# Performance work log

Measured on AMD Instinct MI355X. Metric: run time of the kernel, lower is better.

The kernel has to match this reference:

```python
import jax, jax.numpy as jnp
import numpy as np

B, N, T, D, M, HOPS = 32, 300, 12, 64, 16, 2

def setup_inputs() -> dict:
    key = jax.random.key(0)
    ks = jax.random.split(key, 12)
    inp = {
        "X": jax.random.normal(ks[0], (B, D, N, T), dtype=jnp.float32),
        "timeEmbedding": jax.random.normal(ks[1], (B, N, T, D), dtype=jnp.float32),
        "adjW": jax.random.normal(ks[2], (N, D), dtype=jnp.float32) * (1.0 / np.sqrt(D)),
        "adjB": jnp.zeros((N,), dtype=jnp.float32),
        "trainW1": jax.random.normal(ks[3], (N, M), dtype=jnp.float32) * 0.1,
        "trainW2": jax.random.normal(ks[4], (M, D * D), dtype=jnp.float32) * 0.1,
        "alpha1": jax.random.normal(ks[5], (N, M), dtype=jnp.float32) * 0.1,
        "alpha2": jax.random.normal(ks[6], (M, N), dtype=jnp.float32) * 0.1,
        "beta1": jax.random.normal(ks[7], (N, M), dtype=jnp.float32) * 0.1,
        "beta2": jax.random.normal(ks[8], (M, N), dtype=jnp.float32) * 0.1,
        "gcnW": jax.random.normal(ks[9], (D, D * (HOPS + 1)), dtype=jnp.float32) * (1.0 / np.sqrt(D * (HOPS + 1))),
        "gcnB": jnp.zeros((D,), dtype=jnp.float32),
    }
    return inp

def reference(X, timeEmbedding, adjW, adjB, trainW1, trainW2, alpha1, alpha2, beta1, beta2, gcnW, gcnB):
    # timeEmbedding: [B,N,T,D] -> [B,T,N,D]
    te = jnp.transpose(timeEmbedding, (0, 2, 1, 3))
    # learned adjacency: A[b,t,n,k]
    A = jnp.sin(jnp.einsum('btnd,kd->btnk', te, adjW) + adjB)  # Linear(dmodel->N)
    A = (alpha1 @ alpha2) * A            # elementwise scale by [N,N], broadcast over b,t
    A = jax.nn.relu(A + beta1 @ beta2)
    # X: [B,D,N,T] -> [B,T,N,D]
    Xp = jnp.transpose(X, (0, 3, 2, 1))
    # per-node weight matrices [N,D,D]
    W = (trainW1 @ trainW2).reshape(N, D, D)
    Hs = [Xp]
    Hb = Xp
    for _ in range(HOPS):
        Hnow = jnp.einsum('btnk,btkd->btnd', A, Hb)      # adjacency aggregation
        Hnow = jnp.einsum('btnk,nkd->btnd', Hnow, W)     # per-node distinct matmul
        pre = Xp + Hnow
        Hnow = jax.nn.sigmoid(pre) * jnp.tanh(pre)        # gated residual
        Hs.append(Hnow)
        Hb = Hnow
    H = jnp.concatenate(Hs, axis=3)                       # [B,T,N,D*(hops+1)]
    Hout = jnp.einsum('btnf,df->btnd', H, gcnW) + gcnB    # gcnLinear (dropout = identity in eval)
    return jnp.transpose(Hout, (0, 3, 2, 1))              # [B,D,N,T]
```

## Files before the change

kernel.cpp:

```cpp
#include <hip/hip_runtime.h>

#define Nq 300
#define Tq 12
#define Dq 64
#define Mq 16
#define BTq 384
#define DDq (Dq*Dq)
#define Fq (Dq*3)
#define NP 320

typedef short bf8_t __attribute__((ext_vector_type(8)));
typedef float f4_t  __attribute__((ext_vector_type(4)));

__device__ __forceinline__ unsigned short f2bf(float f) {
    unsigned u = __float_as_uint(f);
    u = (u + 0x7FFFu + ((u >> 16) & 1u)) >> 16;
    return (unsigned short)u;
}
__device__ __forceinline__ float bf2f(unsigned short u) {
    return __uint_as_float((unsigned)u << 16);
}
__device__ __forceinline__ float4 ld4(const float* p) { return *(const float4*)p; }

__device__ __forceinline__ bf8_t pack8(float4 a, float4 b) {
    bf8_t r;
    r[0] = (short)f2bf(a.x); r[1] = (short)f2bf(a.y);
    r[2] = (short)f2bf(a.z); r[3] = (short)f2bf(a.w);
    r[4] = (short)f2bf(b.x); r[5] = (short)f2bf(b.y);
    r[6] = (short)f2bf(b.z); r[7] = (short)f2bf(b.w);
    return r;
}

__device__ __forceinline__ float gatef(float p) {
    float pc = fminf(fmaxf(p, -30.f), 30.f);
    float sig = 1.f / (1.f + __expf(-pc));
    float e2  = __expf(2.f * pc);
    float th  = (e2 - 1.f) / (e2 + 1.f);
    return sig * th;
}

__global__ void __launch_bounds__(256) kprep_all(
    const float* __restrict__ a1, const float* __restrict__ a2,
    const float* __restrict__ b1, const float* __restrict__ b2,
    const float* __restrict__ w1, const float* __restrict__ w2,
    const float* __restrict__ adjW, const float* __restrict__ adjB,
    const float* __restrict__ X,
    unsigned* __restrict__ ABt, unsigned short* __restrict__ Wt,
    unsigned short* __restrict__ adjWb, float* __restrict__ adjBp,
    unsigned short* __restrict__ Xp_t, unsigned short* __restrict__ Xp_nb)
{
    __shared__ char smem[64 * 308 * 2];
    const int vb = blockIdx.x;
    const int tid = threadIdx.x;

    if (vb < 400) {
        const int tile = vb;
        const int reg = tid & 3, lane = tid >> 2;
        const int nt = tile % 5;  int r1 = tile / 5;
        const int w  = r1 % 4;    int r2 = r1 / 4;
        const int c  = r2 % 5;    const int qi = r2 / 5;
        const int n = qi*80 + nt*16 + (lane & 15);
        const int k = c*64 + w*16 + (lane >> 4)*4 + reg;
        unsigned outv = 0u;
        if (n < Nq && k < Nq) {
            float sa = 0.f, sb = 0.f;
            #pragma unroll
            for (int m = 0; m < Mq; ++m) {
                sa = fmaf(a1[n*Mq+m], a2[m*Nq+k], sa);
                sb = fmaf(b1[n*Mq+m], b2[m*Nq+k], sb);
            }
            outv = ((unsigned)f2bf(sb) << 16) | (unsigned)f2bf(sa);
        }
        ABt[tile*256 + tid] = outv;
    } else if (vb < 700) {
        float* sT = (float*)smem;
        __shared__ float sw1[Mq];
        const int n = vb - 400;
        if (tid < Mq) sw1[tid] = w1[n*Mq + tid];
        __syncthreads();
        for (int i = tid; i < DDq; i += 256) {
            int k = i >> 6, d = i & 63;
            float s = 0.f;
            #pragma unroll
            for (int m = 0; m < Mq; ++m) s = fmaf(sw1[m], w2[m*DDq + i], s);
            sT[d*65 + k] = s;
        }
        __syncthreads();
        for (int i = tid; i < DDq; i += 256) {
            int d = i >> 6, k = i & 63;
            Wt[(size_t)n*DDq + i] = f2bf(sT[d*65 + k]);
        }
    } else if (vb < 780) {
        int e = (vb - 700) * 256 + tid;
        if (e < NP * 64) {
            int k = e >> 6, d = e & 63;
            adjWb[e] = (k < Nq) ? f2bf(adjW[k*Dq + d]) : (unsigned short)0;
        }
        if (e < NP) adjBp[e] = (e < Nq) ? adjB[e] : 0.f;
    } else {
        unsigned short* sT = (unsigned short*)smem;
        const int bx = vb - 780;
        const int b = bx / 24, sub = bx % 24;
        const int tile = sub >> 1, half = sub & 1;
        const int n0 = tile * 25, d0 = half * 32;
        for (int i = tid; i < 32 * 75; i += 256) {
            int dl = i / 75, jq = i - dl*75, j = jq*4;
            float4 v = ld4(&X[(size_t)(b*64 + d0 + dl)*3600 + n0*12 + j]);
            ushort4 o;
            o.x = f2bf(v.x); o.y = f2bf(v.y); o.z = f2bf(v.z); o.w = f2bf(v.w);
            *(ushort4*)&sT[dl*308 + j] = o;
        }
        __syncthreads();
        for (int wi = tid; wi < 12 * 32 * 25; wi += 256) {
            int nl = wi % 25, rem = wi / 25;
            int dl = rem & 31, t = rem >> 5;
            Xp_t[((size_t)(b*Tq + t)*64 + d0 + dl)*NP + n0 + nl] = sT[dl*308 + nl*12 + t];
        }
        if (tile == 11) {
            for (int wi = tid; wi < 12 * 32 * 20; wi += 256) {
                int e = wi % 20, rem = wi / 20;
                int dl = rem & 31, t = rem >> 5;
                Xp_t[((size_t)(b*Tq + t)*64 + d0 + dl)*NP + 300 + e] = 0;
            }
        }
        for (int wi = tid; wi < 25 * 12 * 8; wi += 256) {
            int dg = wi & 7, rem = wi >> 3;
            int t = rem % 12, nl = rem / 12;
            ushort4 o;
            o.x = sT[(dg*4+0)*308 + nl*12 + t];
            o.y = sT[(dg*4+1)*308 + nl*12 + t];
            o.z = sT[(dg*4+2)*308 + nl*12 + t];
            o.w = sT[(dg*4+3)*308 + nl*12 + t];
            *(ushort4*)&Xp_nb[((size_t)(n0+nl)*BTq + b*Tq + t)*64 + d0 + dg*4] = o;
        }
    }
}

__global__ void __launch_bounds__(256) ktr2(const unsigned short* __restrict__ Hnb,
                                            unsigned short* __restrict__ Ht) {
    __shared__ unsigned short sT[64 * 308];
    const int bt = blockIdx.x;
    const int tid = threadIdx.x;
    for (int i = tid; i < 300 * 16; i += 256) {
        int nl = i >> 4, dg = i & 15;
        ushort4 v = *(const ushort4*)&Hnb[((size_t)nl*BTq + bt)*64 + dg*4];
        sT[(dg*4+0)*308 + nl] = v.x;
        sT[(dg*4+1)*308 + nl] = v.y;
        sT[(dg*4+2)*308 + nl] = v.z;
        sT[(dg*4+3)*308 + nl] = v.w;
    }
    __syncthreads();
    for (int wi = tid; wi < 64 * 80; wi += 256) {
        int kq = wi % 80, d = wi / 80;
        ushort4 o;
        int k = kq * 4;
        o.x = (k+0 < Nq) ? sT[d*308 + k+0] : (unsigned short)0;
        o.y = (k+1 < Nq) ? sT[d*308 + k+1] : (unsigned short)0;
        o.z = (k+2 < Nq) ? sT[d*308 + k+2] : (unsigned short)0;
        o.w = (k+3 < Nq) ? sT[d*308 + k+3] : (unsigned short)0;
        *(ushort4*)&Ht[((size_t)bt*64 + d)*NP + k] = o;
    }
}

template<int HOP>
__global__ void __launch_bounds__(256) kfuse_t(
    const float* __restrict__ te,
    unsigned short* __restrict__ teP,
    const unsigned short* __restrict__ adjWb,
    const float* __restrict__ adjBp,
    const unsigned* __restrict__ ABt,
    const unsigned short* __restrict__ Hb_t,
    unsigned short* __restrict__ Hout_nb)
{
    __shared__ unsigned short sPl[2][80 * 72];
    const int bt = blockIdx.x >> 2, qi = blockIdx.x & 3;
    const int b = bt / Tq, t = bt - b * Tq;
    const int nbase = qi * 80;
    const int tid = threadIdx.x;
    const int w = tid >> 6, lane = tid & 63, quad = lane >> 4, l16 = lane & 15;
    const int dcol = w*16 + l16;

    bf8_t tb0[5], tb1[5];
    #pragma unroll
    for (int nt = 0; nt < 5; ++nt) {
        int n = nbase + nt*16 + l16; if (n > Nq-1) n = Nq-1;
        if (HOP == 1) {
            const float* ter = te + (((size_t)b*Nq + n)*Tq + t)*Dq;
            tb0[nt] = pack8(ld4(ter + quad*8),      ld4(ter + quad*8 + 4));
            tb1[nt] = pack8(ld4(ter + 32 + quad*8), ld4(ter + 36 + quad*8));
            if (w == 0) {
                *(bf8_t*)&teP[((size_t)bt*Nq + n)*64 + quad*8] = tb0[nt];
                *(bf8_t*)&teP[((size_t)bt*Nq + n)*64 + 32 + quad*8] = tb1[nt];
            }
        } else {
            const unsigned short* tr = teP + ((size_t)bt*Nq + n)*64;
            tb0[nt] = *(const bf8_t*)(tr + quad*8);
            tb1[nt] = *(const bf8_t*)(tr + 32 + quad*8);
        }
    }
    f4_t accO[5];
    #pragma unroll
    for (int rt = 0; rt < 5; ++rt) accO[rt] = (f4_t){0.f, 0.f, 0.f, 0.f};

    const unsigned short* hr = Hb_t + ((size_t)bt*64 + dcol)*NP;
    bf8_t hv0 = *(const bf8_t*)(hr + quad*8);
    bf8_t hv1 = *(const bf8_t*)(hr + 32 + quad*8);

    for (int c = 0; c < 5; ++c) {
        const int cbase = c * 64;
        bf8_t nhv0, nhv1;
        if (c < 4) {
            nhv0 = *(const bf8_t*)(hr + cbase + 64 + quad*8);
            nhv1 = *(const bf8_t*)(hr + cbase + 96 + quad*8);
        }
        const unsigned* abbase = ABt + ((((size_t)qi*5 + c)*4 + w)*5)*256 + lane*4;
        uint4 abv[5];
        #pragma unroll
        for (int nt = 0; nt < 5; ++nt) abv[nt] = *(const uint4*)(abbase + nt*256);
        const unsigned short* ar = adjWb + (cbase + w*16 + l16)*64;
        bf8_t ka0 = *(const bf8_t*)(ar + quad*8);
        bf8_t ka1 = *(const bf8_t*)(ar + 32 + quad*8);
        float4 bias4 = ld4(adjBp + cbase + w*16 + quad*4);
        unsigned short* sp = sPl[c & 1];
        #pragma unroll
        for (int nt = 0; nt < 5; ++nt) {
            f4_t p = {0.f, 0.f, 0.f, 0.f};
            p = __builtin_amdgcn_mfma_f32_16x16x32_bf16(ka0, tb0[nt], p, 0, 0, 0);
            p = __builtin_amdgcn_mfma_f32_16x16x32_bf16(ka1, tb1[nt], p, 0, 0, 0);
            uint4 ab = abv[nt];
            ushort4 o4;
            {
                float sv = __sinf(p[0] + bias4.x);
                o4.x = f2bf(fmaxf(fmaf(__uint_as_float(ab.x << 16), sv,
                                       __uint_as_float(ab.x & 0xFFFF0000u)), 0.f));
            }
            {
                float sv = __sinf(p[1] + bias4.y);
                o4.y = f2bf(fmaxf(fmaf(__uint_as_float(ab.y << 16), sv,
                                       __uint_as_float(ab.y & 0xFFFF0000u)), 0.f));
            }
            {
                float sv = __sinf(p[2] + bias4.z);
                o4.z = f2bf(fmaxf(fmaf(__uint_as_float(ab.z << 16), sv,
                                       __uint_as_float(ab.z & 0xFFFF0000u)), 0.f));
            }
            {
                float sv = __sinf(p[3] + bias4.w);
                o4.w = f2bf(fmaxf(fmaf(__uint_as_float(ab.w << 16), sv,
                                       __uint_as_float(ab.w & 0xFFFF0000u)), 0.f));
            }
            *(ushort4*)&sp[(nt*16 + l16)*72 + w*16 + quad*4] = o4;
        }
        __syncthreads();
        #pragma unroll
        for (int rt = 0; rt < 5; ++rt) {
            bf8_t p0 = *(const bf8_t*)&sp[(rt*16 + l16)*72 + quad*8];
            bf8_t p1 = *(const bf8_t*)&sp[(rt*16 + l16)*72 + 32 + quad*8];
            accO[rt] = __builtin_amdgcn_mfma_f32_16x16x32_bf16(hv0, p0, accO[rt], 0, 0, 0);
            accO[rt] = __builtin_amdgcn_mfma_f32_16x16x32_bf16(hv1, p1, accO[rt], 0, 0, 0);
        }
        if (c < 4) { hv0 = nhv0; hv1 = nhv1; }
    }
    #pragma unroll
    for (int rt = 0; rt < 5; ++rt) {
        int n = nbase + rt*16 + l16;
        if (n < Nq) {
            ushort4 o;
            o.x = f2bf(accO[rt][0]); o.y = f2bf(accO[rt][1]);
            o.z = f2bf(accO[rt][2]); o.w = f2bf(accO[rt][3]);
            *(ushort4*)&Hout_nb[((size_t)n*BTq + bt)*64 + w*16 + quad*4] = o;
        }
    }
}

__global__ void __launch_bounds__(256) kmm(
    const unsigned short* __restrict__ Hagg_nb,
    const unsigned short* __restrict__ Xp_nb,
    const unsigned short* __restrict__ Wt,
    unsigned short* __restrict__ Hout_nb)
{
    const int n = blockIdx.x >> 2, qi = blockIdx.x & 3;
    const int bt0 = qi * 96;
    const int tid = threadIdx.x;
    const int w = tid >> 6, lane = tid & 63, quad = lane >> 4, l16 = lane & 15;
    const int dcol = w*16 + l16;
    const unsigned short* wn = Wt + (size_t)n * DDq + dcol*64;
    bf8_t v0 = *(const bf8_t*)(wn + quad*8);
    bf8_t v1 = *(const bf8_t*)(wn + 32 + quad*8);
    bf8_t a0[6], a1[6];
    #pragma unroll
    for (int rt = 0; rt < 6; ++rt) {
        int r = bt0 + rt*16 + l16;
        const unsigned short* row = Hagg_nb + ((size_t)n*BTq + r)*64;
        a0[rt] = *(const bf8_t*)(row + quad*8);
        a1[rt] = *(const bf8_t*)(row + 32 + quad*8);
    }
    f4_t acc[6];
    #pragma unroll
    for (int rt = 0; rt < 6; ++rt) acc[rt] = (f4_t){0.f, 0.f, 0.f, 0.f};
    #pragma unroll
    for (int rt = 0; rt < 6; ++rt) {
        acc[rt] = __builtin_amdgcn_mfma_f32_16x16x32_bf16(v0, a0[rt], acc[rt], 0, 0, 0);
        acc[rt] = __builtin_amdgcn_mfma_f32_16x16x32_bf16(v1, a1[rt], acc[rt], 0, 0, 0);
    }
    __syncthreads();
    ushort4 xp4[6];
    #pragma unroll
    for (int rt = 0; rt < 6; ++rt) {
        int r = bt0 + rt*16 + l16;
        xp4[rt] = *(const ushort4*)&Xp_nb[((size_t)n*BTq + r)*64 + w*16 + quad*4];
    }
    #pragma unroll
    for (int rt = 0; rt < 6; ++rt) {
        int r = bt0 + rt*16 + l16;
        ushort4 o;
        o.x = f2bf(gatef(bf2f(xp4[rt].x) + acc[rt][0]));
        o.y = f2bf(gatef(bf2f(xp4[rt].y) + acc[rt][1]));
        o.z = f2bf(gatef(bf2f(xp4[rt].z) + acc[rt][2]));
        o.w = f2bf(gatef(bf2f(xp4[rt].w) + acc[rt][3]));
        *(ushort4*)&Hout_nb[((size_t)n*BTq + r)*64 + w*16 + quad*4] = o;
    }
}

__global__ void __launch_bounds__(256) kgcn(
    const unsigned short* __restrict__ Xp_nb, const unsigned short* __restrict__ H1_nb,
    const unsigned short* __restrict__ H2_nb, const float* __restrict__ gcnW,
    const float* __restrict__ gcnB, float* __restrict__ out)
{
    const int bid = blockIdx.x;
    const int b = bid / 57, rem = bid % 57;
    const int tile = rem / 3, rg = rem % 3;
    const int n0 = tile * 16;
    const int rows = (tile == 18) ? 144 : 192;
    const int r0base = rg * 64;
    const int tid = threadIdx.x;
    const int w = tid >> 6, lane = tid & 63, quad = lane >> 4, l16 = lane & 15;
    const int dcol = w*16 + l16;
    const float bias = gcnB[dcol];
    f4_t acc[4];
    #pragma unroll
    for (int rt = 0; rt < 4; ++rt) acc[rt] = (f4_t){0.f, 0.f, 0.f, 0.f};
    const unsigned short* bufs[3] = {Xp_nb, H1_nb, H2_nb};
    #pragma unroll
    for (int c = 0; c < 3; ++c) {
        const unsigned short* buf = bufs[c];
        const float* gwr = gcnW + (size_t)dcol*Fq + c*Dq;
        bf8_t v0 = pack8(ld4(gwr + quad*8),      ld4(gwr + quad*8 + 4));
        bf8_t v1 = pack8(ld4(gwr + 32 + quad*8), ld4(gwr + 36 + quad*8));
        #pragma unroll
        for (int rt = 0; rt < 4; ++rt) {
            int rr = r0base + rt*16;
            if (rr < rows) {
                int r = rr + l16;
                int nl = r / 12, t = r - nl*12;
                int n = n0 + nl; if (n > Nq-1) n = Nq-1;
                const unsigned short* row = buf + ((size_t)n*BTq + b*Tq + t)*64;
                bf8_t a0 = *(const bf8_t*)(row + quad*8);
                bf8_t a1 = *(const bf8_t*)(row + 32 + quad*8);
                acc[rt] = __builtin_amdgcn_mfma_f32_16x16x32_bf16(a0, v0, acc[rt], 0, 0, 0);
                acc[rt] = __builtin_amdgcn_mfma_f32_16x16x32_bf16(a1, v1, acc[rt], 0, 0, 0);
            }
        }
    }
    float* outd = out + (size_t)(b*Dq + dcol)*3600 + n0*12;
    #pragma unroll
    for (int rt = 0; rt < 4; ++rt) {
        int rr = r0base + rt*16;
        if (rr < rows) {
            int r0 = rr + quad*4;
            float4 o = make_float4(acc[rt][0] + bias, acc[rt][1] + bias,
                                   acc[rt][2] + bias, acc[rt][3] + bias);
            *(float4*)&outd[r0] = o;
        }
    }
}

extern "C" void kernel_launch(void* const* d_in, const int* in_sizes, int n_in,
                              void* d_out, int out_size, void* d_ws, size_t ws_size,
                              hipStream_t stream) {
    (void)in_sizes; (void)n_in; (void)out_size; (void)ws_size;
    const float* X    = (const float*)d_in[0];
    const float* te   = (const float*)d_in[1];
    const float* adjW = (const float*)d_in[2];
    const float* adjB = (const float*)d_in[3];
    const float* w1   = (const float*)d_in[4];
    const float* w2   = (const float*)d_in[5];
    const float* a1   = (const float*)d_in[6];
    const float* a2   = (const float*)d_in[7];
    const float* b1   = (const float*)d_in[8];
    const float* b2   = (const float*)d_in[9];
    const float* gW   = (const float*)d_in[10];
    const float* gB   = (const float*)d_in[11];
    float* out = (float*)d_out;

    char* ws = (char*)d_ws;
    unsigned*       ABt    = (unsigned*)      (ws);
    unsigned short* adjWb  = (unsigned short*)(ws + 409600);
    float*          adjBp  = (float*)         (ws + 450560);
    unsigned short* Wt     = (unsigned short*)(ws + 451840);
    unsigned short* Xp_t   = (unsigned short*)(ws + 2909440);
    unsigned short* Xp_nb  = (unsigned short*)(ws + 18638080);
    unsigned short* Hagg   = (unsigned short*)(ws + 33383680);
    unsigned short* H1_nb  = (unsigned short*)(ws + 48129280);
    unsigned short* H1_t   = (unsigned short*)(ws + 62874880);
    unsigned short* teP    = (unsigned short*)(ws + 78603520);

    hipLaunchKernelGGL(kprep_all, dim3(1548), dim3(256), 0, stream,
                       a1, a2, b1, b2, w1, w2, adjW, adjB, X,
                       ABt, Wt, adjWb, adjBp, Xp_t, Xp_nb);
    hipLaunchKernelGGL(HIP_KERNEL_NAME(kfuse_t<1>), dim3(1536), dim3(256), 0, stream,
                       te, teP, adjWb, adjBp, ABt, Xp_t, Hagg);
    hipLaunchKernelGGL(kmm,   dim3(1200), dim3(256), 0, stream, Hagg, Xp_nb, Wt, H1_nb);
    hipLaunchKernelGGL(ktr2,  dim3(384),  dim3(256), 0, stream, H1_nb, H1_t);
    hipLaunchKernelGGL(HIP_KERNEL_NAME(kfuse_t<2>), dim3(1536), dim3(256), 0, stream,
                       te, teP, adjWb, adjBp, ABt, H1_t, Hagg);
    hipLaunchKernelGGL(kmm,   dim3(1200), dim3(256), 0, stream, Hagg, Xp_nb, Wt, Hagg);
    hipLaunchKernelGGL(kgcn,  dim3(1824), dim3(256), 0, stream, Xp_nb, H1_nb, Hagg, gW, gB, out);
}
```

Baseline: 295.9 us.

## Repartition fused adjacency kernel so each wave owns a 16-node tile

The fused adjacency+aggregation kernel now gives each wavefront its own 16-row node tile. Each wave computes all 64 adjacency columns per chunk itself and uses a private shared-memory slice, so the block-wide __syncthreads is gone. The grid grows from 1536 to 1920 blocks to cover 20 node groups per (b,t). The cost is that adjWb rows and the H tile are now loaded by every wave rather than shared across waves, so the H tile is re-read from global memory about four times more often.

```diff
diff --git a/kernel.cpp b/kernel.cpp
--- a/kernel.cpp
+++ b/kernel.cpp
@@ -172,103 +172,98 @@
     const unsigned short* __restrict__ Hb_t,
     unsigned short* __restrict__ Hout_nb)
 {
-    __shared__ unsigned short sPl[2][80 * 72];
-    const int bt = blockIdx.x >> 2, qi = blockIdx.x & 3;
+    __shared__ unsigned short sP[4][16 * 72];
+    const int bt = blockIdx.x / 5, blkq = blockIdx.x % 5;
     const int b = bt / Tq, t = bt - b * Tq;
-    const int nbase = qi * 80;
     const int tid = threadIdx.x;
-    const int w = tid >> 6, lane = tid & 63, quad = lane >> 4, l16 = lane & 15;
-    const int dcol = w*16 + l16;
-
-    bf8_t tb0[5], tb1[5];
-    #pragma unroll
-    for (int nt = 0; nt < 5; ++nt) {
-        int n = nbase + nt*16 + l16; if (n > Nq-1) n = Nq-1;
-        if (HOP == 1) {
-            const float* ter = te + (((size_t)b*Nq + n)*Tq + t)*Dq;
-            tb0[nt] = pack8(ld4(ter + quad*8),      ld4(ter + quad*8 + 4));
-            tb1[nt] = pack8(ld4(ter + 32 + quad*8), ld4(ter + 36 + quad*8));
-            if (w == 0) {
-                *(bf8_t*)&teP[((size_t)bt*Nq + n)*64 + quad*8] = tb0[nt];
-                *(bf8_t*)&teP[((size_t)bt*Nq + n)*64 + 32 + quad*8] = tb1[nt];
-            }
-        } else {
-            const unsigned short* tr = teP + ((size_t)bt*Nq + n)*64;
-            tb0[nt] = *(const bf8_t*)(tr + quad*8);
-            tb1[nt] = *(const bf8_t*)(tr + 32 + quad*8);
-        }
-    }
-    f4_t accO[5];
-    #pragma unroll
-    for (int rt = 0; rt < 5; ++rt) accO[rt] = (f4_t){0.f, 0.f, 0.f, 0.f};
-
-    const unsigned short* hr = Hb_t + ((size_t)bt*64 + dcol)*NP;
-    bf8_t hv0 = *(const bf8_t*)(hr + quad*8);
-    bf8_t hv1 = *(const bf8_t*)(hr + 32 + quad*8);
+    const int wid = tid >> 6, lane = tid & 63, quad = lane >> 4, l16 = lane & 15;
+    const int group = blkq * 4 + wid;
+    const int qi = group / 5, nt = group % 5;
+    const int n0 = group * 16;
+    const int n = n0 + l16;
+    const int nc = (n > Nq-1) ? (Nq-1) : n;
+    unsigned short* sp = sP[wid];
+
+    bf8_t tb0, tb1;
+    if (HOP == 1) {
+        const float* ter = te + (((size_t)b*Nq + nc)*Tq + t)*Dq;
+        tb0 = pack8(ld4(ter + quad*8),      ld4(ter + quad*8 + 4));
+        tb1 = pack8(ld4(ter + 32 + quad*8), ld4(ter + 36 + quad*8));
+        if (n < Nq) {
+            *(bf8_t*)&teP[((size_t)bt*Nq + n)*64 + quad*8] = tb0;
+            *(bf8_t*)&teP[((size_t)bt*Nq + n)*64 + 32 + quad*8] = tb1;
+        }
+    } else {
+        const unsigned short* tr = teP + ((size_t)bt*Nq + nc)*64;
+        tb0 = *(const bf8_t*)(tr + quad*8);
+        tb1 = *(const bf8_t*)(tr + 32 + quad*8);
+    }
+
+    f4_t accO[4];
+    #pragma unroll
+    for (int db = 0; db < 4; ++db) accO[db] = (f4_t){0.f, 0.f, 0.f, 0.f};
+
+    const unsigned short* hrow = Hb_t + (size_t)bt*64*NP;
 
     for (int c = 0; c < 5; ++c) {
         const int cbase = c * 64;
-        bf8_t nhv0, nhv1;
-        if (c < 4) {
-            nhv0 = *(const bf8_t*)(hr + cbase + 64 + quad*8);
-            nhv1 = *(const bf8_t*)(hr + cbase + 96 + quad*8);
-        }
-        const unsigned* abbase = ABt + ((((size_t)qi*5 + c)*4 + w)*5)*256 + lane*4;
-        uint4 abv[5];
+        const unsigned* abq = ABt + ((((size_t)qi*5 + c)*4)*5 + nt)*256 + (quad*16 + l16)*4;
+        uint4 abv[4];
         #pragma unroll
-        for (int nt = 0; nt < 5; ++nt) abv[nt] = *(const uint4*)(abbase + nt*256);
-        const unsigned short* ar = adjWb + (cbase + w*16 + l16)*64;
-        bf8_t ka0 = *(const bf8_t*)(ar + quad*8);
-        bf8_t ka1 = *(const bf8_t*)(ar + 32 + quad*8);
-        float4 bias4 = ld4(adjBp + cbase + w*16 + quad*4);
-        unsigned short* sp = sPl[c & 1];
+        for (int kb = 0; kb < 4; ++kb) abv[kb] = *(const uint4*)(abq + kb*5*256);
+
         #pragma unroll
-        for (int nt = 0; nt < 5; ++nt) {
-            f4_t p = {0.f, 0.f, 0.f, 0.f};
-            p = __builtin_amdgcn_mfma_f32_16x16x32_bf16(ka0, tb0[nt], p, 0, 0, 0);
-            p = __builtin_amdgcn_mfma_f32_16x16x32_bf16(ka1, tb1[nt], p, 0, 0, 0);
-            uint4 ab = abv[nt];
-            ushort4 o4;
+        for (int kb = 0; kb < 4; ++kb) {
+            const unsigned short* ar = adjWb + (cbase + kb*16 + l16)*64;
+            bf8_t ka0 = *(const bf8_t*)(ar + quad*8);
+            bf8_t ka1 = *(const bf8_t*)(ar + 32 + quad*8);
+            f4_t pd = {0.f, 0.f, 0.f, 0.f};
+            pd = __builtin_amdgcn_mfma_f32_16x16x32_bf16(ka0, tb0, pd, 0, 0, 0);
+            pd = __builtin_amdgcn_mfma_f32_16x16x32_bf16(ka1, tb1, pd, 0, 0, 0);
+            float4 bias4 = ld4(adjBp + cbase + kb*16 + quad*4);
+            uint4 ab = abv[kb];
+            unsigned r0, r1, r2, r3;
             {
-                float sv = __sinf(p[0] + bias4.x);
-                o4.x = f2bf(fmaxf(fmaf(__uint_as_float(ab.x << 16), sv,
-                                       __uint_as_float(ab.x & 0xFFFF0000u)), 0.f));
+                float sv = __sinf(pd[0] + bias4.x);
+                r0 = f2bf(fmaxf(fmaf(__uint_as_float(ab.x << 16), sv,
+                                     __uint_as_float(ab.x & 0xFFFF0000u)), 0.f));
             }
             {
-                float sv = __sinf(p[1] + bias4.y);
-                o4.y = f2bf(fmaxf(fmaf(__uint_as_float(ab.y << 16), sv,
-                                       __uint_as_float(ab.y & 0xFFFF0000u)), 0.f));
+                float sv = __sinf(pd[1] + bias4.y);
+                r1 = f2bf(fmaxf(fmaf(__uint_as_float(ab.y << 16), sv,
+                                     __uint_as_float(ab.y & 0xFFFF0000u)), 0.f));
             }
             {
-                float sv = __sinf(p[2] + bias4.z);
-                o4.z = f2bf(fmaxf(fmaf(__uint_as_float(ab.z << 16), sv,
-                                       __uint_as_float(ab.z & 0xFFFF0000u)), 0.f));
+                float sv = __sinf(pd[2] + bias4.z);
+                r2 = f2bf(fmaxf(fmaf(__uint_as_float(ab.z << 16), sv,
+                                     __uint_as_float(ab.z & 0xFFFF0000u)), 0.f));
             }
             {
-                float sv = __sinf(p[3] + bias4.w);
-                o4.w = f2bf(fmaxf(fmaf(__uint_as_float(ab.w << 16), sv,
-                                       __uint_as_float(ab.w & 0xFFFF0000u)), 0.f));
-            }
-            *(ushort4*)&sp[(nt*16 + l16)*72 + w*16 + quad*4] = o4;
-        }
-        __syncthreads();
+                float sv = __sinf(pd[3] + bias4.w);
+                r3 = f2bf(fmaxf(fmaf(__uint_as_float(ab.w << 16), sv,
+                                     __uint_as_float(ab.w & 0xFFFF0000u)), 0.f));
+            }
+            *(uint2*)&sp[l16*72 + kb*16 + quad*4] =
+                make_uint2((r1 << 16) | r0, (r3 << 16) | r2);
+        }
+        bf8_t pb0 = *(const bf8_t*)&sp[l16*72 + quad*8];
+        bf8_t pb1 = *(const bf8_t*)&sp[l16*72 + 32 + quad*8];
         #pragma unroll
-        for (int rt = 0; rt < 5; ++rt) {
-            bf8_t p0 = *(const bf8_t*)&sp[(rt*16 + l16)*72 + quad*8];
-            bf8_t p1 = *(const bf8_t*)&sp[(rt*16 + l16)*72 + 32 + quad*8];
-            accO[rt] = __builtin_amdgcn_mfma_f32_16x16x32_bf16(hv0, p0, accO[rt], 0, 0, 0);
-            accO[rt] = __builtin_amdgcn_mfma_f32_16x16x32_bf16(hv1, p1, accO[rt], 0, 0, 0);
-        }
-        if (c < 4) { hv0 = nhv0; hv1 = nhv1; }
-    }
-    #pragma unroll
-    for (int rt = 0; rt < 5; ++rt) {
-        int n = nbase + rt*16 + l16;
-        if (n < Nq) {
+        for (int db = 0; db < 4; ++db) {
+            const unsigned short* hr = hrow + (size_t)(db*16 + l16)*NP + cbase;
+            bf8_t hv0 = *(const bf8_t*)(hr + quad*8);
+            bf8_t hv1 = *(const bf8_t*)(hr + 32 + quad*8);
+            accO[db] = __builtin_amdgcn_mfma_f32_16x16x32_bf16(hv0, pb0, accO[db], 0, 0, 0);
+            accO[db] = __builtin_amdgcn_mfma_f32_16x16x32_bf16(hv1, pb1, accO[db], 0, 0, 0);
+        }
+    }
+    if (n < Nq) {
+        #pragma unroll
+        for (int db = 0; db < 4; ++db) {
             ushort4 o;
-            o.x = f2bf(accO[rt][0]); o.y = f2bf(accO[rt][1]);
-            o.z = f2bf(accO[rt][2]); o.w = f2bf(accO[rt][3]);
-            *(ushort4*)&Hout_nb[((size_t)n*BTq + bt)*64 + w*16 + quad*4] = o;
+            o.x = f2bf(accO[db][0]); o.y = f2bf(accO[db][1]);
+            o.z = f2bf(accO[db][2]); o.w = f2bf(accO[db][3]);
+            *(ushort4*)&Hout_nb[((size_t)n*BTq + bt)*64 + db*16 + quad*4] = o;
         }
     }
 }
@@ -408,11 +403,11 @@
     hipLaunchKernelGGL(kprep_all, dim3(1548), dim3(256), 0, stream,
                        a1, a2, b1, b2, w1, w2, adjW, adjB, X,
                        ABt, Wt, adjWb, adjBp, Xp_t, Xp_nb);
-    hipLaunchKernelGGL(HIP_KERNEL_NAME(kfuse_t<1>), dim3(1536), dim3(256), 0, stream,
+    hipLaunchKernelGGL(HIP_KERNEL_NAME(kfuse_t<1>), dim3(1920), dim3(256), 0, stream,
                        te, teP, adjWb, adjBp, ABt, Xp_t, Hagg);
     hipLaunchKernelGGL(kmm,   dim3(1200), dim3(256), 0, stream, Hagg, Xp_nb, Wt, H1_nb);
     hipLaunchKernelGGL(ktr2,  dim3(384),  dim3(256), 0, stream, H1_nb, H1_t);
-    hipLaunchKernelGGL(HIP_KERNEL_NAME(kfuse_t<2>), dim3(1536), dim3(256), 0, stream,
+    hipLaunchKernelGGL(HIP_KERNEL_NAME(kfuse_t<2>), dim3(1920), dim3(256), 0, stream,
                        te, teP, adjWb, adjBp, ABt, H1_t, Hagg);
     hipLaunchKernelGGL(kmm,   dim3(1200), dim3(256), 0, stream, Hagg, Xp_nb, Wt, Hagg);
     hipLaunchKernelGGL(kgcn,  dim3(1824), dim3(256), 0, stream, Xp_nb, H1_nb, Hagg, gW, gB, out);
```

New measurement: 388.9 us. +31.4%, slower.
